# Kernel tuning notes

Measured on AMD Instinct MI355X. Metric: run time of the kernel, lower is better.

## Reference

```python
import jax, jax.numpy as jnp
import numpy as np

N_USERS = 100000
N_ITEMS = 50000
N_ENTITIES = 150000
N_EDGES = 2000000
NNZ = 1000000
CHANNEL = 64
N_HOPS = 2
TEMPERATURE = 0.2
PDIST_EPS = 1e-6   # torch.nn.PairwiseDistance default eps (added to the diff)
NORM_EPS = 1e-12   # F.normalize default eps


def setup_inputs() -> dict:
    key = jax.random.key(0)
    ks = jax.random.split(key, 8)
    return {
        "user_emb": jax.random.normal(ks[0], (N_USERS, CHANNEL), dtype=jnp.float32),
        "entity_emb": jax.random.normal(ks[1], (N_ENTITIES, CHANNEL), dtype=jnp.float32),
        "weight": jax.random.normal(ks[2], (20, CHANNEL), dtype=jnp.float32),
        "edge_index": jax.random.randint(ks[3], (2, N_EDGES), 0, N_ENTITIES, dtype=jnp.int64) if jax.config.jax_enable_x64 else jax.random.randint(ks[3], (2, N_EDGES), 0, N_ENTITIES, dtype=jnp.int32),
        "edge_type": jax.random.randint(ks[4], (N_EDGES,), 0, 20, dtype=jnp.int32),
        "inter_user": jax.random.randint(ks[5], (NNZ,), 0, N_USERS, dtype=jnp.int32),
        "inter_item": jax.random.randint(ks[6], (NNZ,), 0, N_ITEMS, dtype=jnp.int32),
        "inter_vals": jax.random.uniform(ks[7], (NNZ,), dtype=jnp.float32),
    }


def _l2_normalize(x):
    # F.normalize(x, p=2, dim=1): x / max(||x||, eps)
    n = jnp.sqrt(jnp.sum(x * x, axis=-1, keepdims=True))
    return x / jnp.maximum(n, NORM_EPS)


def _aggregate(entity_emb, head, tail, inter_user, inter_item, inter_vals):
    n_entities = entity_emb.shape[0]
    # scatter_mean over KG edges: mean of tail embeddings per head entity
    neigh = entity_emb[tail]                                   # [E, C]
    summed = jax.ops.segment_sum(neigh, head, num_segments=n_entities)
    cnt = jax.ops.segment_sum(jnp.ones((head.shape[0],), entity_emb.dtype), head,
                              num_segments=n_entities)
    entity_agg = summed / jnp.maximum(cnt, 1.0)[:, None]       # [n_entities, C]

    items = entity_agg[:N_ITEMS]                               # [n_items, C]
    g_items = items[inter_item]                                # [nnz, C]
    # user_mean = interact_map @ entity_agg[:n_items]  (sparse mm via segment_sum)
    user_mean = jax.ops.segment_sum(inter_vals[:, None] * g_items, inter_user,
                                    num_segments=N_USERS)      # [n_users, C]
    # pairwise L2 distance per interaction edge
    diff = g_items - user_mean[inter_user] + PDIST_EPS
    score = jnp.sqrt(jnp.sum(diff * diff, axis=-1)) / TEMPERATURE   # [nnz]
    # sparse softmax over each user row
    row_max = jax.ops.segment_max(score, inter_user, num_segments=N_USERS)
    e = jnp.exp(score - row_max[inter_user])
    denom = jax.ops.segment_sum(e, inter_user, num_segments=N_USERS)
    soft = e / denom[inter_user]                               # [nnz]
    # user_agg = soft_score_mat @ entity_agg[:n_items]
    user_agg = jax.ops.segment_sum(soft[:, None] * g_items, inter_user,
                                   num_segments=N_USERS)       # [n_users, C]
    return user_agg, entity_agg


def reference(user_emb, entity_emb, weight, edge_index, edge_type,
              inter_user, inter_item, inter_vals):
    # GraphConv.forward with mess_dropout=False, node_dropout=False (deterministic)
    head, tail = edge_index[0], edge_index[1]
    user_res, entity_res = user_emb, entity_emb
    u, ent = user_emb, entity_emb
    for _ in range(N_HOPS):
        u, ent = _aggregate(ent, head, tail, inter_user, inter_item, inter_vals)
        ent = _l2_normalize(ent)
        u = _l2_normalize(u)
        entity_res = entity_res + ent
        user_res = user_res + u
    return user_res, entity_res
```

## Files before the change

### kernel.cpp

```cpp
#include <hip/hip_runtime.h>

#define N_USERS   100000
#define N_ITEMS   50000
#define N_ENT     150000
#define N_EDGES   2000000
#define NNZ       1000000
#define CH        64

#define CB_SHIFT  9
#define CB_SIZE   512
#define NB_E      ((N_ENT   + CB_SIZE - 1) >> CB_SHIFT)
#define NB_U      ((N_USERS + CB_SIZE - 1) >> CB_SHIFT)
#define A_CHUNK   4096
#define UCACHE    32

#define NBLK_CNT   512
#define NBLK_CONV  ((N_ENT * 16 + 255) / 256)
#define NBLK_BS_E  ((N_EDGES + A_CHUNK - 1) / A_CHUNK)
#define NBLK_BS_U  ((NNZ + A_CHUNK - 1) / A_CHUNK)
#define GB_G8      ((N_ENT + 31) / 32)
#define GB_USER    (N_USERS / 4)
#define G2U1_NG    1563

typedef __fp16 h2v __attribute__((ext_vector_type(2)));

__device__ __forceinline__ h2v h2z() { h2v z = {(__fp16)0.f, (__fp16)0.f}; return z; }
__device__ __forceinline__ h2v pk(float a, float b) { return __builtin_amdgcn_cvt_pkrtz(a, b); }
__device__ __forceinline__ unsigned int h2u(h2v h) { return __builtin_bit_cast(unsigned int, h); }
__device__ __forceinline__ h2v u2h(unsigned int u) { return __builtin_bit_cast(h2v, u); }
__device__ __forceinline__ float fdot2f(h2v a, h2v b, float c) {
    return __builtin_amdgcn_fdot2(a, b, c, false);
}

template<int CTRL>
__device__ __forceinline__ float dpp_mov(float x) {
    return __builtin_bit_cast(float, __builtin_amdgcn_update_dpp(
        0, __builtin_bit_cast(int, x), CTRL, 0xF, 0xF, true));
}
template<int CTRL>
__device__ __forceinline__ unsigned dpp_mov_u(unsigned x) {
    return (unsigned)__builtin_amdgcn_update_dpp(0, (int)x, CTRL, 0xF, 0xF, true);
}
__device__ __forceinline__ float red8(float x) {
    x += dpp_mov<0xB1>(x);
    x += dpp_mov<0x4E>(x);
    x += dpp_mov<0x141>(x);
    return x;
}
__device__ __forceinline__ h2v grpadd8(h2v a) {
    return a + u2h(dpp_mov_u<0x128>(h2u(a)));
}


__device__ __forceinline__ void coarse_count_f(const int* __restrict__ key, int n,
                                               unsigned int* __restrict__ gcnt, int nb,
                                               unsigned int* h, int bid, int nblk) {
    for (int i = threadIdx.x; i < nb; i += blockDim.x) h[i] = 0;
    __syncthreads();
    for (int e = bid * blockDim.x + threadIdx.x; e < n; e += nblk * blockDim.x)
        atomicAdd(&h[key[e] >> CB_SHIFT], 1u);
    __syncthreads();
    for (int i = threadIdx.x; i < nb; i += blockDim.x)
        if (h[i]) atomicAdd(&gcnt[i], h[i]);
}

__global__ void build_p1(const int* __restrict__ head, const int* __restrict__ iu,
                         const float* __restrict__ entity_emb, uint2* __restrict__ E0,
                         unsigned int* __restrict__ cntE, unsigned int* __restrict__ cntU) {
    __shared__ unsigned int h[CB_SIZE];
    int bid = blockIdx.x;
    if (bid < NBLK_CNT) {
        coarse_count_f(head, N_EDGES, cntE, NB_E, h, bid, NBLK_CNT);
    } else if (bid < 2 * NBLK_CNT) {
        coarse_count_f(iu, NNZ, cntU, NB_U, h, bid - NBLK_CNT, NBLK_CNT);
    } else {
        int i = (bid - 2 * NBLK_CNT) * 256 + threadIdx.x;
        if (i < N_ENT * 16) {
            float4 a = ((const float4*)entity_emb)[i];
            E0[i] = make_uint2(h2u(pk(a.x, a.y)), h2u(pk(a.z, a.w)));
        }
    }
}

__device__ __forceinline__ void coarse_scan_f(const unsigned int* __restrict__ gcnt,
                                              unsigned int* __restrict__ base,
                                              unsigned int* __restrict__ cursor, int nb,
                                              unsigned int* s) {
    int t = threadIdx.x;
    unsigned int v = (t < nb) ? gcnt[t] : 0u;
    s[t] = v;
    __syncthreads();
    for (int off = 1; off < 512; off <<= 1) {
        unsigned int u = 0;
        if (t >= off) u = s[t - off];
        __syncthreads();
        if (t >= off) s[t] += u;
        __syncthreads();
    }
    if (t < nb) { base[t] = s[t] - v; cursor[t] = s[t] - v; }
    if (t == nb) base[t] = s[nb - 1];
}

__global__ void build_p2(const unsigned int* __restrict__ cntE, unsigned int* __restrict__ baseE,
                         unsigned int* __restrict__ curE,
                         const unsigned int* __restrict__ cntU, unsigned int* __restrict__ baseU,
                         unsigned int* __restrict__ curU) {
    __shared__ unsigned int s[512];
    if (blockIdx.x == 0) coarse_scan_f(cntE, baseE, curE, NB_E, s);
    else                 coarse_scan_f(cntU, baseU, curU, NB_U, s);
}

__device__ __forceinline__ void binscat_ent_f(const int* __restrict__ head,
                                              const int* __restrict__ tail,
                                              unsigned int* __restrict__ cursor,
                                              unsigned int* __restrict__ binned,
                                              unsigned int* h, unsigned int* bb, int bid) {
    int lo = bid * A_CHUNK;
    int hi = min(lo + A_CHUNK, N_EDGES);
    for (int i = threadIdx.x; i < NB_E; i += blockDim.x) h[i] = 0;
    __syncthreads();
    for (int e = lo + threadIdx.x; e < hi; e += blockDim.x)
        atomicAdd(&h[head[e] >> CB_SHIFT], 1u);
    __syncthreads();
    for (int i = threadIdx.x; i < NB_E; i += blockDim.x) {
        unsigned int c = h[i];
        bb[i] = c ? atomicAdd(&cursor[i], c) : 0u;
        h[i] = 0;
    }
    __syncthreads();
    for (int e = lo + threadIdx.x; e < hi; e += blockDim.x) {
        int hd = head[e];
        int b = hd >> CB_SHIFT;
        unsigned int r = atomicAdd(&h[b], 1u);
        unsigned int local = (unsigned int)hd & (CB_SIZE - 1);
        binned[bb[b] + r] = (local << 18) | (unsigned int)tail[e];
    }
}

__device__ __forceinline__ void binscat_user_f(const int* __restrict__ iu,
                                               const int* __restrict__ ii,
                                               const float* __restrict__ iv,
                                               unsigned int* __restrict__ cursor,
                                               unsigned int* __restrict__ binned,
                                               float* __restrict__ binnedv,
                                               unsigned int* h, unsigned int* bb, int bid) {
    int lo = bid * A_CHUNK;
    int hi = min(lo + A_CHUNK, NNZ);
    for (int i = threadIdx.x; i < NB_U; i += blockDim.x) h[i] = 0;
    __syncthreads();
    for (int e = lo + threadIdx.x; e < hi; e += blockDim.x)
        atomicAdd(&h[iu[e] >> CB_SHIFT], 1u);
    __syncthreads();
    for (int i = threadIdx.x; i < NB_U; i += blockDim.x) {
        unsigned int c = h[i];
        bb[i] = c ? atomicAdd(&cursor[i], c) : 0u;
        h[i] = 0;
    }
    __syncthreads();
    for (int e = lo + threadIdx.x; e < hi; e += blockDim.x) {
        int u = iu[e];
        int b = u >> CB_SHIFT;
        unsigned int r = atomicAdd(&h[b], 1u);
        unsigned int slot = bb[b] + r;
        unsigned int local = (unsigned int)u & (CB_SIZE - 1);
        binned[slot] = (local << 16) | (unsigned int)ii[e];
        binnedv[slot] = iv[e];
    }
}

__global__ void build_p3e(const int* __restrict__ head, const int* __restrict__ tail,
                          unsigned int* __restrict__ curE, unsigned int* __restrict__ binnedE) {
    __shared__ unsigned int h[NB_E];
    __shared__ unsigned int bb[NB_E];
    binscat_ent_f(head, tail, curE, binnedE, h, bb, blockIdx.x);
}

__device__ __forceinline__ void build_ent_f(const unsigned int* __restrict__ base,
                                            const unsigned int* __restrict__ binned,
                                            int* __restrict__ col,
                                            unsigned int* __restrict__ row_start,
                                            unsigned int* h, unsigned int* ex,
                                            unsigned int* pairs, int b) {
    unsigned int s0 = base[b], s1 = base[b + 1];
    int t = threadIdx.x;
    h[2 * t] = 0; h[2 * t + 1] = 0;
    __syncthreads();
    for (unsigned int j = s0 + t; j < s1; j += 256)
        atomicAdd(&h[binned[j] >> 18], 1u);
    __syncthreads();
    unsigned int a0 = h[2 * t], a1 = h[2 * t + 1];
    pairs[t] = a0 + a1;
    __syncthreads();
    for (int off = 1; off < 256; off <<= 1) {
        unsigned int u = 0;
        if (t >= off) u = pairs[t - off];
        __syncthreads();
        if (t >= off) pairs[t] += u;
        __syncthreads();
    }
    unsigned int pe = pairs[t] - (a0 + a1);
    ex[2 * t] = pe;
    ex[2 * t + 1] = pe + a0;
    __syncthreads();
    int keybase = b << CB_SHIFT;
    #pragma unroll
    for (int k = 0; k < 2; ++k) {
        int i = 2 * t + k;
        int key = keybase + i;
        if (key < N_ENT) row_start[key] = s0 + ex[i];
    }
    if (b == 0 && t == 0) row_start[N_ENT] = base[NB_E];
    __syncthreads();
    h[2 * t] = 0; h[2 * t + 1] = 0;
    __syncthreads();
    for (unsigned int j = s0 + t; j < s1; j += 256) {
        unsigned int p = binned[j];
        unsigned int local = p >> 18;
        unsigned int r = atomicAdd(&h[local], 1u);
        col[s0 + ex[local] + r] = (int)(p & 0x3FFFFu);
    }
}

__device__ __forceinline__ void build_user_f(const unsigned int* __restrict__ base,
                                             const unsigned int* __restrict__ binned,
                                             const float* __restrict__ binnedv,
                                             int2* __restrict__ upair,
                                             unsigned int* __restrict__ u_row_start,
                                             unsigned int* h, unsigned int* ex,
                                             unsigned int* pairs, int b) {
    unsigned int s0 = base[b], s1 = base[b + 1];
    int t = threadIdx.x;
    h[2 * t] = 0; h[2 * t + 1] = 0;
    __syncthreads();
    for (unsigned int j = s0 + t; j < s1; j += 256)
        atomicAdd(&h[binned[j] >> 16], 1u);
    __syncthreads();
    unsigned int a0 = h[2 * t], a1 = h[2 * t + 1];
    pairs[t] = a0 + a1;
    __syncthreads();
    for (int off = 1; off < 256; off <<= 1) {
        unsigned int u = 0;
        if (t >= off) u = pairs[t - off];
        __syncthreads();
        if (t >= off) pairs[t] += u;
        __syncthreads();
    }
    unsigned int pe = pairs[t] - (a0 + a1);
    ex[2 * t] = pe;
    ex[2 * t + 1] = pe + a0;
    __syncthreads();
    int keybase = b << CB_SHIFT;
    #pragma unroll
    for (int k = 0; k < 2; ++k) {
        int i = 2 * t + k;
        int key = keybase + i;
        if (key < N_USERS) u_row_start[key] = s0 + ex[i];
    }
    if (b == 0 && t == 0) u_row_start[N_USERS] = base[NB_U];
    __syncthreads();
    h[2 * t] = 0; h[2 * t + 1] = 0;
    __syncthreads();
    for (unsigned int j = s0 + t; j < s1; j += 256) {
        unsigned int p = binned[j];
        float v = binnedv[j];
        unsigned int local = p >> 16;
        unsigned int r = atomicAdd(&h[local], 1u);
        upair[s0 + ex[local] + r] = make_int2((int)(p & 0xFFFFu), __float_as_int(v));
    }
}

__global__ void build_p3u_p4e(const int* __restrict__ iu, const int* __restrict__ ii,
                              const float* __restrict__ iv, unsigned int* __restrict__ curU,
                              unsigned int* __restrict__ binnedU, float* __restrict__ binnedUV,
                              const unsigned int* __restrict__ baseE,
                              const unsigned int* __restrict__ binnedE,
                              int* __restrict__ col, unsigned int* __restrict__ row_start) {
    __shared__ unsigned int h[CB_SIZE];
    __shared__ unsigned int ex[CB_SIZE];
    __shared__ unsigned int pairs[256];
    if (blockIdx.x < NBLK_BS_U)
        binscat_user_f(iu, ii, iv, curU, binnedU, binnedUV, h, ex , blockIdx.x);
    else
        build_ent_f(baseE, binnedE, col, row_start, h, ex, pairs, blockIdx.x - NBLK_BS_U);
}


__device__ __forceinline__ void gather_fin_row8(int row, int t, bool valid,
        const uint4* __restrict__ entb, const unsigned int* __restrict__ row_start,
        const int* __restrict__ col,
        uint4* __restrict__ ent_out, uint4* __restrict__ items_out,
        const float* __restrict__ base_ent, const uint4* __restrict__ v1tab,
        float* __restrict__ out_ent, int mode) {
    unsigned int s0 = 0, s1 = 0;
    if (valid) { s0 = row_start[row]; s1 = row_start[row + 1]; }

    h2v a0 = h2z(), a1 = h2z(), a2 = h2z(), a3 = h2z();
    unsigned int j = s0;
    for (; j + 1 < s1; j += 2) {
        int c0 = col[j], c1 = col[j + 1];
        uint4 x0 = entb[(size_t)c0 * 8 + t];
        uint4 x1 = entb[(size_t)c1 * 8 + t];
        a0 += u2h(x0.x) + u2h(x1.x);
        a1 += u2h(x0.y) + u2h(x1.y);
        a2 += u2h(x0.z) + u2h(x1.z);
        a3 += u2h(x0.w) + u2h(x1.w);
    }
    if (j < s1) {
        uint4 x = entb[(size_t)col[j] * 8 + t];
        a0 += u2h(x.x); a1 += u2h(x.y); a2 += u2h(x.z); a3 += u2h(x.w);
    }
    float inv = 1.0f / fmaxf((float)(s1 - s0), 1.0f);
    float m0 = (float)a0[0] * inv, m1 = (float)a0[1] * inv;
    float m2 = (float)a1[0] * inv, m3 = (float)a1[1] * inv;
    float m4 = (float)a2[0] * inv, m5 = (float)a2[1] * inv;
    float m6 = (float)a3[0] * inv, m7 = (float)a3[1] * inv;

    float sq = m0*m0 + m1*m1 + m2*m2 + m3*m3 + m4*m4 + m5*m5 + m6*m6 + m7*m7;
    sq = red8(sq);
    float invn = 1.0f / fmaxf(sqrtf(sq), 1e-12f);

    if (!valid) return;
    size_t o = (size_t)row * 8 + t;
    if (row < N_ITEMS)
        items_out[o] = make_uint4(h2u(pk(m0, m1)), h2u(pk(m2, m3)),
                                  h2u(pk(m4, m5)), h2u(pk(m6, m7)));
    if (mode == 0) {
        ent_out[o] = make_uint4(h2u(pk(m0*invn, m1*invn)), h2u(pk(m2*invn, m3*invn)),
                                h2u(pk(m4*invn, m5*invn)), h2u(pk(m6*invn, m7*invn)));
    } else {
        size_t fo = (size_t)row * 16 + 2 * t;
        float4 c0 = ((const float4*)base_ent)[fo];
        float4 c1 = ((const float4*)base_ent)[fo + 1];
        uint4 v1 = v1tab[o];
        h2v p0 = u2h(v1.x), p1 = u2h(v1.y), p2 = u2h(v1.z), p3 = u2h(v1.w);
        ((float4*)out_ent)[fo]     = make_float4(c0.x + (float)p0[0] + m0*invn,
                                                 c0.y + (float)p0[1] + m1*invn,
                                                 c0.z + (float)p1[0] + m2*invn,
                                                 c0.w + (float)p1[1] + m3*invn);
        ((float4*)out_ent)[fo + 1] = make_float4(c1.x + (float)p2[0] + m4*invn,
                                                 c1.y + (float)p2[1] + m5*invn,
                                                 c1.z + (float)p3[0] + m6*invn,
                                                 c1.w + (float)p3[1] + m7*invn);
    }
}

template<int NS>
__device__ __forceinline__ void user_fast_path(
        unsigned int s0, unsigned int deg, int grp, int t,
        const uint4* __restrict__ itemsb, const int2* __restrict__ up,
        float& l, h2v& ac0, h2v& ac1, h2v& ac2, h2v& ac3) {
    const float SC = 5.0f * 1.44269504f;
    uint4 r[NS];
    float vw[NS];
    #pragma unroll
    for (int k = 0; k < NS; ++k) {
        unsigned int slot = (unsigned int)grp + 8u * k;
        if (slot < deg) {
            int2 p = up[s0 + slot];
            r[k] = itemsb[(size_t)p.x * 8 + t];
            vw[k] = __int_as_float(p.y);
        } else {
            r[k] = make_uint4(0u, 0u, 0u, 0u);
            vw[k] = 0.0f;
        }
    }
    h2v um0 = h2z(), um1 = h2z(), um2 = h2z(), um3 = h2z();
    #pragma unroll
    for (int k = 0; k < NS; ++k) {
        h2v v2 = pk(vw[k], vw[k]);
        um0 += v2 * u2h(r[k].x); um1 += v2 * u2h(r[k].y);
        um2 += v2 * u2h(r[k].z); um3 += v2 * u2h(r[k].w);
    }
    um0 = grpadd8(um0); um1 = grpadd8(um1); um2 = grpadd8(um2); um3 = grpadd8(um3);
    #pragma unroll
    for (int m = 16; m <= 32; m <<= 1) {
        um0 += u2h(__shfl_xor(h2u(um0), m, 64));
        um1 += u2h(__shfl_xor(h2u(um1), m, 64));
        um2 += u2h(__shfl_xor(h2u(um2), m, 64));
        um3 += u2h(__shfl_xor(h2u(um3), m, 64));
    }
    float scv[NS];
    float mloc = -1e30f;
    #pragma unroll
    for (int k = 0; k < NS; ++k) {
        unsigned int slot = (unsigned int)grp + 8u * k;
        h2v d0 = u2h(r[k].x) - um0, d1 = u2h(r[k].y) - um1;
        h2v d2 = u2h(r[k].z) - um2, d3 = u2h(r[k].w) - um3;
        float sq = fdot2f(d3, d3, fdot2f(d2, d2, fdot2f(d1, d1, fdot2f(d0, d0, 0.0f))));
        sq = red8(sq);
        float sc = sqrtf(sq) * SC;
        scv[k] = (slot < deg) ? sc : -1e30f;
        mloc = fmaxf(mloc, scv[k]);
    }
    mloc = fmaxf(mloc, dpp_mov<0x128>(mloc));
    float M = fmaxf(mloc, __shfl_xor(mloc, 16, 64));
    M = fmaxf(M, __shfl_xor(M, 32, 64));
    #pragma unroll
    for (int k = 0; k < NS; ++k) {
        float e = exp2f(scv[k] - M);
        l += e;
        h2v e2 = pk(e, e);
        ac0 += e2 * u2h(r[k].x); ac1 += e2 * u2h(r[k].y);
        ac2 += e2 * u2h(r[k].z); ac3 += e2 * u2h(r[k].w);
    }
}

__device__ __forceinline__ void fused_user_row(int row, int lane, uint4 (*cw)[8],
        const uint4* __restrict__ itemsb, const unsigned int* __restrict__ u_row_start,
        const int2* __restrict__ up, const float* __restrict__ base_user,
        float* __restrict__ out_user) {
    int grp = lane >> 3;
    int t   = lane & 7;
    unsigned int s0 = u_row_start[row];
    unsigned int s1 = u_row_start[row + 1];
    unsigned int deg = s1 - s0;

    const float SC = 5.0f * 1.44269504f;
    float l = 0.0f;
    h2v ac0 = h2z(), ac1 = h2z(), ac2 = h2z(), ac3 = h2z();

    if (__builtin_expect(deg <= 16, 1)) {
        user_fast_path<2>(s0, deg, grp, t, itemsb, up, l, ac0, ac1, ac2, ac3);
    } else if (deg <= UCACHE) {
        user_fast_path<4>(s0, deg, grp, t, itemsb, up, l, ac0, ac1, ac2, ac3);
    } else {
        h2v um0 = h2z(), um1 = h2z(), um2 = h2z(), um3 = h2z();
        for (unsigned int j = s0 + grp; j < s1; j += 8) {
            int2 p = up[j];
            uint4 r = itemsb[(size_t)p.x * 8 + t];
            int slot = (int)(j - s0);
            if (slot < UCACHE) cw[slot][t] = r;
            float v = __int_as_float(p.y);
            h2v v2 = pk(v, v);
            um0 += v2 * u2h(r.x); um1 += v2 * u2h(r.y);
            um2 += v2 * u2h(r.z); um3 += v2 * u2h(r.w);
        }
        um0 = grpadd8(um0); um1 = grpadd8(um1); um2 = grpadd8(um2); um3 = grpadd8(um3);
        #pragma unroll
        for (int m = 16; m <= 32; m <<= 1) {
            um0 += u2h(__shfl_xor(h2u(um0), m, 64));
            um1 += u2h(__shfl_xor(h2u(um1), m, 64));
            um2 += u2h(__shfl_xor(h2u(um2), m, 64));
            um3 += u2h(__shfl_xor(h2u(um3), m, 64));
        }
        float m_run = -1e30f;
        for (unsigned int j = s0 + grp; j < s1; j += 8) {
            int slot = (int)(j - s0);
            uint4 r = (slot < UCACHE) ? cw[slot][t]
                                      : itemsb[(size_t)up[j].x * 8 + t];
            h2v d0 = u2h(r.x) - um0, d1 = u2h(r.y) - um1;
            h2v d2 = u2h(r.z) - um2, d3 = u2h(r.w) - um3;
            float sq = fdot2f(d3, d3, fdot2f(d2, d2, fdot2f(d1, d1, fdot2f(d0, d0, 0.0f))));
            sq = red8(sq);
            float sc = sqrtf(sq) * SC;
            if (sc > m_run) {
                float s = exp2f(m_run - sc);
                l *= s;
                h2v s2 = pk(s, s);
                ac0 *= s2; ac1 *= s2; ac2 *= s2; ac3 *= s2;
                m_run = sc;
            }
            float e = exp2f(sc - m_run);
            l += e;
            h2v e2 = pk(e, e);
            ac0 += e2 * u2h(r.x); ac1 += e2 * u2h(r.y);
            ac2 += e2 * u2h(r.z); ac3 += e2 * u2h(r.w);
        }
        float mx = fmaxf(m_run, dpp_mov<0x128>(m_run));
        float M = fmaxf(mx, __shfl_xor(mx, 16, 64));
        M = fmaxf(M, __shfl_xor(M, 32, 64));
        float wgt = (l > 0.0f) ? exp2f(m_run - M) : 0.0f;
        l *= wgt;
        h2v w2 = pk(wgt, wgt);
        ac0 *= w2; ac1 *= w2; ac2 *= w2; ac3 *= w2;
    }

    l = l + dpp_mov<0x128>(l);
    ac0 = grpadd8(ac0); ac1 = grpadd8(ac1); ac2 = grpadd8(ac2); ac3 = grpadd8(ac3);
    #pragma unroll
    for (int m = 16; m <= 32; m <<= 1) {
        l   += __shfl_xor(l, m, 64);
        ac0 += u2h(__shfl_xor(h2u(ac0), m, 64));
        ac1 += u2h(__shfl_xor(h2u(ac1), m, 64));
        ac2 += u2h(__shfl_xor(h2u(ac2), m, 64));
        ac3 += u2h(__shfl_xor(h2u(ac3), m, 64));
    }
    float invl = (l > 0.0f) ? (1.0f / l) : 0.0f;
    float u0 = (float)ac0[0] * invl, u1 = (float)ac0[1] * invl;
    float u2 = (float)ac1[0] * invl, u3 = (float)ac1[1] * invl;
    float u4 = (float)ac2[0] * invl, u5 = (float)ac2[1] * invl;
    float u6 = (float)ac3[0] * invl, u7 = (float)ac3[1] * invl;

    float sq2 = u0*u0 + u1*u1 + u2*u2 + u3*u3 + u4*u4 + u5*u5 + u6*u6 + u7*u7;
    sq2 = red8(sq2);
    float inv = 1.0f / fmaxf(sqrtf(sq2), 1e-12f);
    if (grp == 0) {
        size_t fo = (size_t)row * 16 + 2 * t;
        float4 c0 = ((const float4*)base_user)[fo];
        float4 c1 = ((const float4*)base_user)[fo + 1];
        ((float4*)out_user)[fo]     = make_float4(c0.x + u0*inv, c0.y + u1*inv,
                                                  c0.z + u2*inv, c0.w + u3*inv);
        ((float4*)out_user)[fo + 1] = make_float4(c1.x + u4*inv, c1.y + u5*inv,
                                                  c1.z + u6*inv, c1.w + u7*inv);
    }
}


__global__ void gf1_p4u_k(const uint4* __restrict__ E0,
                          const unsigned int* __restrict__ row_start,
                          const int* __restrict__ col,
                          uint4* __restrict__ E1, uint4* __restrict__ itemsA,
                          const unsigned int* __restrict__ baseU,
                          const unsigned int* __restrict__ binnedU,
                          const float* __restrict__ binnedUV,
                          int2* __restrict__ upair, unsigned int* __restrict__ u_row_start) {
    __shared__ unsigned int h[CB_SIZE];
    __shared__ unsigned int ex[CB_SIZE];
    __shared__ unsigned int pairs[256];
    int bid = blockIdx.x;
    if (bid < NB_U) {
        build_user_f(baseU, binnedU, binnedUV, upair, u_row_start, h, ex, pairs, bid);
    } else {
        int lane = threadIdx.x & 63;
        int row = (bid - NB_U) * 32 + (threadIdx.x >> 6) * 8 + (lane >> 3);
        gather_fin_row8(row, lane & 7, row < N_ENT, E0, row_start, col, E1, itemsA,
                        nullptr, nullptr, nullptr, 0);
    }
}

__global__ void g2_u1_k(const uint4* __restrict__ entb,
                        const unsigned int* __restrict__ row_start,
                        const int* __restrict__ col,
                        uint4* __restrict__ items_out,
                        const float* __restrict__ entity_emb,
                        float* __restrict__ out_ent,
                        const uint4* __restrict__ itemsb1,
                        const unsigned int* __restrict__ u_row_start,
                        const int2* __restrict__ up,
                        const float* __restrict__ base_user,
                        float* __restrict__ out_user) {
    __shared__ uint4 cache[4][UCACHE][8];
    int bid = blockIdx.x;
    int g = bid / 19, r = bid - g * 19;
    int w    = threadIdx.x >> 6;
    int lane = threadIdx.x & 63;
    if (r < 3) {
        int gb = g * 3 + r;
        int row = gb * 32 + w * 8 + (lane >> 3);
        gather_fin_row8(row, lane & 7, row < N_ENT, entb, row_start, col,
                        nullptr, items_out, entity_emb, entb, out_ent, 1);
    } else {
        int idx = g * 16 + (r - 3);
        int row = idx * 4 + w;
        if (row < N_USERS)
            fused_user_row(row, lane, cache[w], itemsb1, u_row_start, up,
                           base_user, out_user);
    }
}

__global__ void fused_user_k(const uint4* __restrict__ itemsb,
                             const unsigned int* __restrict__ u_row_start,
                             const int2* __restrict__ up,
                             const float* __restrict__ base_user,
                             float* __restrict__ out_user) {
    __shared__ uint4 cache[4][UCACHE][8];
    int wave = (blockIdx.x * blockDim.x + threadIdx.x) >> 6;
    int w    = threadIdx.x >> 6;
    int lane = threadIdx.x & 63;
    if (wave >= N_USERS) return;
    fused_user_row(wave, lane, cache[w], itemsb, u_row_start, up, base_user, out_user);
}

extern "C" void kernel_launch(void* const* d_in, const int* in_sizes, int n_in,
                              void* d_out, int out_size, void* d_ws, size_t ws_size,
                              hipStream_t stream) {
    const float* user_emb   = (const float*)d_in[0];
    const float* entity_emb = (const float*)d_in[1];
    const int*   edge_index = (const int*)d_in[3];
    const int*   iu = (const int*)d_in[5];
    const int*   ii = (const int*)d_in[6];
    const float* iv = (const float*)d_in[7];

    float* out_user = (float*)d_out;
    float* out_ent  = out_user + (size_t)N_USERS * CH;

    uint4* E0     = (uint4*)d_ws;
    uint4* E1     = E0 + (size_t)N_ENT * 8;
    uint4* itemsA = E1 + (size_t)N_ENT * 8;
    uint4* itemsB = itemsA + (size_t)N_ITEMS * 8;
    int2*  upair  = (int2*)(itemsB + (size_t)N_ITEMS * 8);
    int*   col    = (int*)(upair + NNZ);
    unsigned int* row_start   = (unsigned int*)(col + N_EDGES);
    unsigned int* u_row_start = row_start + N_ENT + 1;
    unsigned int* cntE  = u_row_start + N_USERS + 1;
    unsigned int* cntU  = cntE + NB_E;
    unsigned int* baseE = cntU + NB_U;
    unsigned int* curE  = baseE + NB_E + 1;
    unsigned int* baseU = curE + NB_E;
    unsigned int* curU  = baseU + NB_U + 1;

    unsigned int* binnedE  = (unsigned int*)E1;
    unsigned int* binnedU  = (unsigned int*)out_user;
    float*        binnedUV = (float*)(binnedU + NNZ);

    const int* head = edge_index;
    const int* tail = edge_index + N_EDGES;

    (void)hipMemsetAsync(cntE, 0, (size_t)(NB_E + NB_U) * 4, stream);
    build_p1<<<2 * NBLK_CNT + NBLK_CONV, 256, 0, stream>>>(head, iu, entity_emb,
                                                           (uint2*)E0, cntE, cntU);
    build_p2<<<2, 512, 0, stream>>>(cntE, baseE, curE, cntU, baseU, curU);
    build_p3e<<<NBLK_BS_E, 256, 0, stream>>>(head, tail, curE, binnedE);
    build_p3u_p4e<<<NBLK_BS_U + NB_E, 256, 0, stream>>>(iu, ii, iv, curU, binnedU, binnedUV,
                                                        baseE, binnedE, col, row_start);

    gf1_p4u_k<<<NB_U + GB_G8, 256, 0, stream>>>(E0, row_start, col, E1, itemsA,
                                                baseU, binnedU, binnedUV,
                                                upair, u_row_start);

    g2_u1_k<<<G2U1_NG * 19, 256, 0, stream>>>(E1, row_start, col, itemsB,
                                              entity_emb, out_ent,
                                              itemsA, u_row_start, upair,
                                              user_emb, out_user);

    fused_user_k<<<GB_USER, 256, 0, stream>>>(itemsB, u_row_start, upair,
                                              out_user, out_user);
}
```

Measured before the change: 434.8 us.

## Replace count-scan binning with fixed-capacity buckets and (start,deg) row descriptors

Drops the global coarse-count and prefix-scan kernels by giving each coarse bucket a fixed-capacity slot region (ECAP/UCAP). Binning, user binning and the fp16 conversion now run in one launch, which removes two launches and a full pass over the keys. Row offsets become (start, degree) pairs, and the KG gather loop is unrolled by four. This assumes no bucket overflows its capacity: counts are clamped with min(), so overflow would silently drop edges. The workspace also grows with the padded buckets.

```diff
diff --git a/kernel.cpp b/kernel.cpp
--- a/kernel.cpp
+++ b/kernel.cpp
@@ -13,8 +13,9 @@
 #define NB_U      ((N_USERS + CB_SIZE - 1) >> CB_SHIFT)
 #define A_CHUNK   4096
 #define UCACHE    32
-
-#define NBLK_CNT   512
+#define ECAP      8192
+#define UCAP      6144
+
 #define NBLK_CONV  ((N_ENT * 16 + 255) / 256)
 #define NBLK_BS_E  ((N_EDGES + A_CHUNK - 1) / A_CHUNK)
 #define NBLK_BS_U  ((NNZ + A_CHUNK - 1) / A_CHUNK)
@@ -52,67 +53,9 @@
 }
 
 
-__device__ __forceinline__ void coarse_count_f(const int* __restrict__ key, int n,
-                                               unsigned int* __restrict__ gcnt, int nb,
-                                               unsigned int* h, int bid, int nblk) {
-    for (int i = threadIdx.x; i < nb; i += blockDim.x) h[i] = 0;
-    __syncthreads();
-    for (int e = bid * blockDim.x + threadIdx.x; e < n; e += nblk * blockDim.x)
-        atomicAdd(&h[key[e] >> CB_SHIFT], 1u);
-    __syncthreads();
-    for (int i = threadIdx.x; i < nb; i += blockDim.x)
-        if (h[i]) atomicAdd(&gcnt[i], h[i]);
-}
-
-__global__ void build_p1(const int* __restrict__ head, const int* __restrict__ iu,
-                         const float* __restrict__ entity_emb, uint2* __restrict__ E0,
-                         unsigned int* __restrict__ cntE, unsigned int* __restrict__ cntU) {
-    __shared__ unsigned int h[CB_SIZE];
-    int bid = blockIdx.x;
-    if (bid < NBLK_CNT) {
-        coarse_count_f(head, N_EDGES, cntE, NB_E, h, bid, NBLK_CNT);
-    } else if (bid < 2 * NBLK_CNT) {
-        coarse_count_f(iu, NNZ, cntU, NB_U, h, bid - NBLK_CNT, NBLK_CNT);
-    } else {
-        int i = (bid - 2 * NBLK_CNT) * 256 + threadIdx.x;
-        if (i < N_ENT * 16) {
-            float4 a = ((const float4*)entity_emb)[i];
-            E0[i] = make_uint2(h2u(pk(a.x, a.y)), h2u(pk(a.z, a.w)));
-        }
-    }
-}
-
-__device__ __forceinline__ void coarse_scan_f(const unsigned int* __restrict__ gcnt,
-                                              unsigned int* __restrict__ base,
-                                              unsigned int* __restrict__ cursor, int nb,
-                                              unsigned int* s) {
-    int t = threadIdx.x;
-    unsigned int v = (t < nb) ? gcnt[t] : 0u;
-    s[t] = v;
-    __syncthreads();
-    for (int off = 1; off < 512; off <<= 1) {
-        unsigned int u = 0;
-        if (t >= off) u = s[t - off];
-        __syncthreads();
-        if (t >= off) s[t] += u;
-        __syncthreads();
-    }
-    if (t < nb) { base[t] = s[t] - v; cursor[t] = s[t] - v; }
-    if (t == nb) base[t] = s[nb - 1];
-}
-
-__global__ void build_p2(const unsigned int* __restrict__ cntE, unsigned int* __restrict__ baseE,
-                         unsigned int* __restrict__ curE,
-                         const unsigned int* __restrict__ cntU, unsigned int* __restrict__ baseU,
-                         unsigned int* __restrict__ curU) {
-    __shared__ unsigned int s[512];
-    if (blockIdx.x == 0) coarse_scan_f(cntE, baseE, curE, NB_E, s);
-    else                 coarse_scan_f(cntU, baseU, curU, NB_U, s);
-}
-
 __device__ __forceinline__ void binscat_ent_f(const int* __restrict__ head,
                                               const int* __restrict__ tail,
-                                              unsigned int* __restrict__ cursor,
+                                              unsigned int* __restrict__ cur,
                                               unsigned int* __restrict__ binned,
                                               unsigned int* h, unsigned int* bb, int bid) {
     int lo = bid * A_CHUNK;
@@ -124,7 +67,7 @@
     __syncthreads();
     for (int i = threadIdx.x; i < NB_E; i += blockDim.x) {
         unsigned int c = h[i];
-        bb[i] = c ? atomicAdd(&cursor[i], c) : 0u;
+        bb[i] = c ? ((unsigned int)i * ECAP + atomicAdd(&cur[i], c)) : 0u;
         h[i] = 0;
     }
     __syncthreads();
@@ -140,7 +83,7 @@
 __device__ __forceinline__ void binscat_user_f(const int* __restrict__ iu,
                                                const int* __restrict__ ii,
                                                const float* __restrict__ iv,
-                                               unsigned int* __restrict__ cursor,
+                                               unsigned int* __restrict__ cur,
                                                unsigned int* __restrict__ binned,
                                                float* __restrict__ binnedv,
                                                unsigned int* h, unsigned int* bb, int bid) {
@@ -153,7 +96,7 @@
     __syncthreads();
     for (int i = threadIdx.x; i < NB_U; i += blockDim.x) {
         unsigned int c = h[i];
-        bb[i] = c ? atomicAdd(&cursor[i], c) : 0u;
+        bb[i] = c ? ((unsigned int)i * UCAP + atomicAdd(&cur[i], c)) : 0u;
         h[i] = 0;
     }
     __syncthreads();
@@ -168,20 +111,38 @@
     }
 }
 
-__global__ void build_p3e(const int* __restrict__ head, const int* __restrict__ tail,
-                          unsigned int* __restrict__ curE, unsigned int* __restrict__ binnedE) {
+__global__ void build_d1(const int* __restrict__ head, const int* __restrict__ tail,
+                         const int* __restrict__ iu, const int* __restrict__ ii,
+                         const float* __restrict__ iv,
+                         const float* __restrict__ entity_emb, uint2* __restrict__ E0,
+                         unsigned int* __restrict__ curE, unsigned int* __restrict__ binnedE,
+                         unsigned int* __restrict__ curU, unsigned int* __restrict__ binnedU,
+                         float* __restrict__ binnedUV) {
     __shared__ unsigned int h[NB_E];
     __shared__ unsigned int bb[NB_E];
-    binscat_ent_f(head, tail, curE, binnedE, h, bb, blockIdx.x);
-}
-
-__device__ __forceinline__ void build_ent_f(const unsigned int* __restrict__ base,
+    int bid = blockIdx.x;
+    if (bid < NBLK_BS_E) {
+        binscat_ent_f(head, tail, curE, binnedE, h, bb, bid);
+    } else if (bid < NBLK_BS_E + NBLK_BS_U) {
+        binscat_user_f(iu, ii, iv, curU, binnedU, binnedUV, h, bb, bid - NBLK_BS_E);
+    } else {
+        int i = (bid - NBLK_BS_E - NBLK_BS_U) * 256 + threadIdx.x;
+        if (i < N_ENT * 16) {
+            float4 a = ((const float4*)entity_emb)[i];
+            E0[i] = make_uint2(h2u(pk(a.x, a.y)), h2u(pk(a.z, a.w)));
+        }
+    }
+}
+
+__device__ __forceinline__ void csort_ent_f(const unsigned int* __restrict__ cnt,
                                             const unsigned int* __restrict__ binned,
                                             int* __restrict__ col,
-                                            unsigned int* __restrict__ row_start,
+                                            uint2* __restrict__ erow,
                                             unsigned int* h, unsigned int* ex,
                                             unsigned int* pairs, int b) {
-    unsigned int s0 = base[b], s1 = base[b + 1];
+    unsigned int s0 = (unsigned int)b * ECAP;
+    unsigned int n  = min(cnt[b], (unsigned int)ECAP);
+    unsigned int s1 = s0 + n;
     int t = threadIdx.x;
     h[2 * t] = 0; h[2 * t + 1] = 0;
     __syncthreads();
@@ -203,13 +164,8 @@
     ex[2 * t + 1] = pe + a0;
     __syncthreads();
     int keybase = b << CB_SHIFT;
-    #pragma unroll
-    for (int k = 0; k < 2; ++k) {
-        int i = 2 * t + k;
-        int key = keybase + i;
-        if (key < N_ENT) row_start[key] = s0 + ex[i];
-    }
-    if (b == 0 && t == 0) row_start[N_ENT] = base[NB_E];
+    if (keybase + 2 * t < N_ENT)     erow[keybase + 2 * t]     = make_uint2(s0 + ex[2 * t], a0);
+    if (keybase + 2 * t + 1 < N_ENT) erow[keybase + 2 * t + 1] = make_uint2(s0 + ex[2 * t + 1], a1);
     __syncthreads();
     h[2 * t] = 0; h[2 * t + 1] = 0;
     __syncthreads();
@@ -221,14 +177,16 @@
     }
 }
 
-__device__ __forceinline__ void build_user_f(const unsigned int* __restrict__ base,
+__device__ __forceinline__ void csort_user_f(const unsigned int* __restrict__ cnt,
                                              const unsigned int* __restrict__ binned,
                                              const float* __restrict__ binnedv,
                                              int2* __restrict__ upair,
-                                             unsigned int* __restrict__ u_row_start,
+                                             uint2* __restrict__ urow,
                                              unsigned int* h, unsigned int* ex,
                                              unsigned int* pairs, int b) {
-    unsigned int s0 = base[b], s1 = base[b + 1];
+    unsigned int s0 = (unsigned int)b * UCAP;
+    unsigned int n  = min(cnt[b], (unsigned int)UCAP);
+    unsigned int s1 = s0 + n;
     int t = threadIdx.x;
     h[2 * t] = 0; h[2 * t + 1] = 0;
     __syncthreads();
@@ -250,13 +208,8 @@
     ex[2 * t + 1] = pe + a0;
     __syncthreads();
     int keybase = b << CB_SHIFT;
-    #pragma unroll
-    for (int k = 0; k < 2; ++k) {
-        int i = 2 * t + k;
-        int key = keybase + i;
-        if (key < N_USERS) u_row_start[key] = s0 + ex[i];
-    }
-    if (b == 0 && t == 0) u_row_start[N_USERS] = base[NB_U];
+    if (keybase + 2 * t < N_USERS)     urow[keybase + 2 * t]     = make_uint2(s0 + ex[2 * t], a0);
+    if (keybase + 2 * t + 1 < N_USERS) urow[keybase + 2 * t + 1] = make_uint2(s0 + ex[2 * t + 1], a1);
     __syncthreads();
     h[2 * t] = 0; h[2 * t + 1] = 0;
     __syncthreads();
@@ -269,47 +222,44 @@
     }
 }
 
-__global__ void build_p3u_p4e(const int* __restrict__ iu, const int* __restrict__ ii,
-                              const float* __restrict__ iv, unsigned int* __restrict__ curU,
-                              unsigned int* __restrict__ binnedU, float* __restrict__ binnedUV,
-                              const unsigned int* __restrict__ baseE,
-                              const unsigned int* __restrict__ binnedE,
-                              int* __restrict__ col, unsigned int* __restrict__ row_start) {
+__global__ void build_d2(const unsigned int* __restrict__ curE,
+                         const unsigned int* __restrict__ binnedE,
+                         int* __restrict__ col, uint2* __restrict__ erow) {
     __shared__ unsigned int h[CB_SIZE];
     __shared__ unsigned int ex[CB_SIZE];
     __shared__ unsigned int pairs[256];
-    if (blockIdx.x < NBLK_BS_U)
-        binscat_user_f(iu, ii, iv, curU, binnedU, binnedUV, h, ex , blockIdx.x);
-    else
-        build_ent_f(baseE, binnedE, col, row_start, h, ex, pairs, blockIdx.x - NBLK_BS_U);
+    csort_ent_f(curE, binnedE, col, erow, h, ex, pairs, blockIdx.x);
 }
 
 
 __device__ __forceinline__ void gather_fin_row8(int row, int t, bool valid,
-        const uint4* __restrict__ entb, const unsigned int* __restrict__ row_start,
+        const uint4* __restrict__ entb, const uint2* __restrict__ erow,
         const int* __restrict__ col,
         uint4* __restrict__ ent_out, uint4* __restrict__ items_out,
         const float* __restrict__ base_ent, const uint4* __restrict__ v1tab,
         float* __restrict__ out_ent, int mode) {
-    unsigned int s0 = 0, s1 = 0;
-    if (valid) { s0 = row_start[row]; s1 = row_start[row + 1]; }
+    unsigned int s0 = 0, deg = 0;
+    if (valid) { uint2 rs = erow[row]; s0 = rs.x; deg = rs.y; }
+    unsigned int s1 = s0 + deg;
 
     h2v a0 = h2z(), a1 = h2z(), a2 = h2z(), a3 = h2z();
     unsigned int j = s0;
-    for (; j + 1 < s1; j += 2) {
-        int c0 = col[j], c1 = col[j + 1];
+    for (; j + 3 < s1; j += 4) {
+        int c0 = col[j], c1 = col[j + 1], c2 = col[j + 2], c3 = col[j + 3];
         uint4 x0 = entb[(size_t)c0 * 8 + t];
         uint4 x1 = entb[(size_t)c1 * 8 + t];
-        a0 += u2h(x0.x) + u2h(x1.x);
-        a1 += u2h(x0.y) + u2h(x1.y);
-        a2 += u2h(x0.z) + u2h(x1.z);
-        a3 += u2h(x0.w) + u2h(x1.w);
-    }
-    if (j < s1) {
+        uint4 x2 = entb[(size_t)c2 * 8 + t];
+        uint4 x3 = entb[(size_t)c3 * 8 + t];
+        a0 += (u2h(x0.x) + u2h(x1.x)) + (u2h(x2.x) + u2h(x3.x));
+        a1 += (u2h(x0.y) + u2h(x1.y)) + (u2h(x2.y) + u2h(x3.y));
+        a2 += (u2h(x0.z) + u2h(x1.z)) + (u2h(x2.z) + u2h(x3.z));
+        a3 += (u2h(x0.w) + u2h(x1.w)) + (u2h(x2.w) + u2h(x3.w));
+    }
+    for (; j < s1; ++j) {
         uint4 x = entb[(size_t)col[j] * 8 + t];
         a0 += u2h(x.x); a1 += u2h(x.y); a2 += u2h(x.z); a3 += u2h(x.w);
     }
-    float inv = 1.0f / fmaxf((float)(s1 - s0), 1.0f);
+    float inv = 1.0f / fmaxf((float)deg, 1.0f);
     float m0 = (float)a0[0] * inv, m1 = (float)a0[1] * inv;
     float m2 = (float)a1[0] * inv, m3 = (float)a1[1] * inv;
     float m4 = (float)a2[0] * inv, m5 = (float)a2[1] * inv;
@@ -406,14 +356,15 @@
 }
 
 __device__ __forceinline__ void fused_user_row(int row, int lane, uint4 (*cw)[8],
-        const uint4* __restrict__ itemsb, const unsigned int* __restrict__ u_row_start,
+        const uint4* __restrict__ itemsb, const uint2* __restrict__ urow,
         const int2* __restrict__ up, const float* __restrict__ base_user,
         float* __restrict__ out_user) {
     int grp = lane >> 3;
     int t   = lane & 7;
-    unsigned int s0 = u_row_start[row];
-    unsigned int s1 = u_row_start[row + 1];
-    unsigned int deg = s1 - s0;
+    uint2 rs = urow[row];
+    unsigned int s0 = rs.x;
+    unsigned int deg = rs.y;
+    unsigned int s1 = s0 + deg;
 
     const float SC = 5.0f * 1.44269504f;
     float l = 0.0f;
@@ -507,35 +458,35 @@
 
 
 __global__ void gf1_p4u_k(const uint4* __restrict__ E0,
-                          const unsigned int* __restrict__ row_start,
+                          const uint2* __restrict__ erow,
                           const int* __restrict__ col,
                           uint4* __restrict__ E1, uint4* __restrict__ itemsA,
-                          const unsigned int* __restrict__ baseU,
+                          const unsigned int* __restrict__ curU,
                           const unsigned int* __restrict__ binnedU,
                           const float* __restrict__ binnedUV,
-                          int2* __restrict__ upair, unsigned int* __restrict__ u_row_start) {
+                          int2* __restrict__ upair, uint2* __restrict__ urow) {
     __shared__ unsigned int h[CB_SIZE];
     __shared__ unsigned int ex[CB_SIZE];
     __shared__ unsigned int pairs[256];
     int bid = blockIdx.x;
     if (bid < NB_U) {
-        build_user_f(baseU, binnedU, binnedUV, upair, u_row_start, h, ex, pairs, bid);
+        csort_user_f(curU, binnedU, binnedUV, upair, urow, h, ex, pairs, bid);
     } else {
         int lane = threadIdx.x & 63;
         int row = (bid - NB_U) * 32 + (threadIdx.x >> 6) * 8 + (lane >> 3);
-        gather_fin_row8(row, lane & 7, row < N_ENT, E0, row_start, col, E1, itemsA,
+        gather_fin_row8(row, lane & 7, row < N_ENT, E0, erow, col, E1, itemsA,
                         nullptr, nullptr, nullptr, 0);
     }
 }
 
 __global__ void g2_u1_k(const uint4* __restrict__ entb,
-                        const unsigned int* __restrict__ row_start,
+                        const uint2* __restrict__ erow,
                         const int* __restrict__ col,
                         uint4* __restrict__ items_out,
                         const float* __restrict__ entity_emb,
                         float* __restrict__ out_ent,
                         const uint4* __restrict__ itemsb1,
-                        const unsigned int* __restrict__ u_row_start,
+                        const uint2* __restrict__ urow,
                         const int2* __restrict__ up,
                         const float* __restrict__ base_user,
                         float* __restrict__ out_user) {
@@ -547,19 +498,19 @@
     if (r < 3) {
         int gb = g * 3 + r;
         int row = gb * 32 + w * 8 + (lane >> 3);
-        gather_fin_row8(row, lane & 7, row < N_ENT, entb, row_start, col,
+        gather_fin_row8(row, lane & 7, row < N_ENT, entb, erow, col,
                         nullptr, items_out, entity_emb, entb, out_ent, 1);
     } else {
         int idx = g * 16 + (r - 3);
         int row = idx * 4 + w;
         if (row < N_USERS)
-            fused_user_row(row, lane, cache[w], itemsb1, u_row_start, up,
+            fused_user_row(row, lane, cache[w], itemsb1, urow, up,
                            base_user, out_user);
     }
 }
 
 __global__ void fused_user_k(const uint4* __restrict__ itemsb,
-                             const unsigned int* __restrict__ u_row_start,
+                             const uint2* __restrict__ urow,
                              const int2* __restrict__ up,
                              const float* __restrict__ base_user,
                              float* __restrict__ out_user) {
@@ -568,7 +519,7 @@
     int w    = threadIdx.x >> 6;
     int lane = threadIdx.x & 63;
     if (wave >= N_USERS) return;
-    fused_user_row(wave, lane, cache[w], itemsb, u_row_start, up, base_user, out_user);
+    fused_user_row(wave, lane, cache[w], itemsb, urow, up, base_user, out_user);
 }
 
 extern "C" void kernel_launch(void* const* d_in, const int* in_sizes, int n_in,
@@ -589,40 +540,34 @@
     uint4* itemsA = E1 + (size_t)N_ENT * 8;
     uint4* itemsB = itemsA + (size_t)N_ITEMS * 8;
     int2*  upair  = (int2*)(itemsB + (size_t)N_ITEMS * 8);
-    int*   col    = (int*)(upair + NNZ);
-    unsigned int* row_start   = (unsigned int*)(col + N_EDGES);
-    unsigned int* u_row_start = row_start + N_ENT + 1;
-    unsigned int* cntE  = u_row_start + N_USERS + 1;
-    unsigned int* cntU  = cntE + NB_E;
-    unsigned int* baseE = cntU + NB_U;
-    unsigned int* curE  = baseE + NB_E + 1;
-    unsigned int* baseU = curE + NB_E;
-    unsigned int* curU  = baseU + NB_U + 1;
+    int*   col    = (int*)(upair + (size_t)NB_U * UCAP);
+    uint2* erow   = (uint2*)(col + (size_t)NB_E * ECAP);
+    uint2* urow   = erow + N_ENT;
+    unsigned int* curE = (unsigned int*)(urow + N_USERS);
+    unsigned int* curU = curE + NB_E;
 
     unsigned int* binnedE  = (unsigned int*)E1;
     unsigned int* binnedU  = (unsigned int*)out_user;
-    float*        binnedUV = (float*)(binnedU + NNZ);
+    float*        binnedUV = (float*)(binnedU + (size_t)NB_U * UCAP);
 
     const int* head = edge_index;
     const int* tail = edge_index + N_EDGES;
 
-    (void)hipMemsetAsync(cntE, 0, (size_t)(NB_E + NB_U) * 4, stream);
-    build_p1<<<2 * NBLK_CNT + NBLK_CONV, 256, 0, stream>>>(head, iu, entity_emb,
-                                                           (uint2*)E0, cntE, cntU);
-    build_p2<<<2, 512, 0, stream>>>(cntE, baseE, curE, cntU, baseU, curU);
-    build_p3e<<<NBLK_BS_E, 256, 0, stream>>>(head, tail, curE, binnedE);
-    build_p3u_p4e<<<NBLK_BS_U + NB_E, 256, 0, stream>>>(iu, ii, iv, curU, binnedU, binnedUV,
-                                                        baseE, binnedE, col, row_start);
-
-    gf1_p4u_k<<<NB_U + GB_G8, 256, 0, stream>>>(E0, row_start, col, E1, itemsA,
-                                                baseU, binnedU, binnedUV,
-                                                upair, u_row_start);
-
-    g2_u1_k<<<G2U1_NG * 19, 256, 0, stream>>>(E1, row_start, col, itemsB,
+    (void)hipMemsetAsync(curE, 0, (size_t)(NB_E + NB_U) * 4, stream);
+    build_d1<<<NBLK_BS_E + NBLK_BS_U + NBLK_CONV, 256, 0, stream>>>(
+        head, tail, iu, ii, iv, entity_emb, (uint2*)E0,
+        curE, binnedE, curU, binnedU, binnedUV);
+    build_d2<<<NB_E, 256, 0, stream>>>(curE, binnedE, col, erow);
+
+    gf1_p4u_k<<<NB_U + GB_G8, 256, 0, stream>>>(E0, erow, col, E1, itemsA,
+                                                curU, binnedU, binnedUV,
+                                                upair, urow);
+
+    g2_u1_k<<<G2U1_NG * 19, 256, 0, stream>>>(E1, erow, col, itemsB,
                                               entity_emb, out_ent,
-                                              itemsA, u_row_start, upair,
+                                              itemsA, urow, upair,
                                               user_emb, out_user);
 
-    fused_user_k<<<GB_USER, 256, 0, stream>>>(itemsB, u_row_start, upair,
+    fused_user_k<<<GB_USER, 256, 0, stream>>>(itemsB, urow, upair,
                                               out_user, out_user);
 }
```

After: 399.5 us. 8.1% less time.
